# Optimization experiments

Measured on AMD Instinct MI355X. Metric: run time of the kernel, lower is better.

## Reference

```python
import jax, jax.numpy as jnp
import numpy as np
from jax import lax

B, C, T, D, H, W = 1, 8, 8, 24, 48, 48
KT = 3  # temporal kernel taps (module's time loop == valid forward conv, stride 1, pad 0)
KS = 3  # spatial kernel size
S = 2   # spatial stride of the transposed conv
P = 1   # spatial padding of the transposed conv


def setup_inputs() -> dict:
    key = jax.random.key(0)
    kx, kw = jax.random.split(key)
    x = jax.random.normal(kx, (B, C, T, D, H, W), dtype=jnp.float32)
    # torch layout (out_channels, in_channels, kT, kD, kH, kW); the module assigns the
    # slice weight[:, :, i] directly as ConvTranspose3d.weight, so at runtime dim0 acts
    # as the transpose-conv INPUT-channel dim (works because in_ch == out_ch).
    fan_in = C * KT * KS ** 3
    bound = float(1.0 / np.sqrt(fan_in))
    weight = jax.random.uniform(kw, (C, C, KT, KS, KS, KS), dtype=jnp.float32,
                                minval=-bound, maxval=bound)
    return {"x": x, "weight": weight}


def _convT3d(x5, wt):
    # x5: [N, Cin, D, H, W]; wt: ConvTranspose3d weight laid out [Cin, Cout, kD, kH, kW].
    # Transposed conv == forward conv with spatially flipped kernel, swapped I/O dims,
    # lhs dilation = stride, per-side padding = dil*(k-1) - p.
    rhs = jnp.flip(wt, axis=(2, 3, 4)).transpose(1, 0, 2, 3, 4)  # [Cout, Cin, k, k, k]
    pad = KS - 1 - P
    return lax.conv_general_dilated(
        x5, rhs,
        window_strides=(1, 1, 1),
        padding=[(pad, pad)] * 3,
        lhs_dilation=(S, S, S),
        dimension_numbers=("NCDHW", "OIDHW", "NCDHW"))


def reference(x, weight):
    b, c, t = x.shape[:3]
    t_o = t - (KT - 1)  # temporal valid forward conv: out[f] = sum_i conv_i(x[f + i])
    # fold time into batch so each temporal tap is a single big 3D conv
    xr = x.transpose(0, 2, 1, 3, 4, 5).reshape(b * t, c, *x.shape[3:])
    out = None
    for i in range(KT):  # small fixed loop over kernel taps
        y = _convT3d(xr, weight[:, :, i])                 # [b*t, C, Do, Ho, Wo]
        y = y.reshape(b, t, *y.shape[1:])[:, i:i + t_o]   # frames x[f+i] -> out[f]
        out = y if out is None else out + y
    return out.transpose(0, 2, 1, 3, 4, 5)  # [B, C, t_o, Do, Ho, Wo]
```

## Files before the change

### kernel.cpp

```cpp
#include <hip/hip_runtime.h>


typedef float  f32x4  __attribute__((ext_vector_type(4)));
typedef float  f4a    __attribute__((ext_vector_type(4)));
typedef short  bf16x8 __attribute__((ext_vector_type(8)));
typedef unsigned int u32;
typedef u32    u32x2  __attribute__((ext_vector_type(2)));
typedef u32    u32x4  __attribute__((ext_vector_type(4)));

namespace {
constexpr int T_ = 8, D_ = 24, H_ = 48, W_ = 48;
constexpr int TO = 6, DO_ = 47, HO = 95, WO = 95;
constexpr int XCS = T_ * D_ * H_ * W_;
constexpr int XFS = D_ * H_ * W_;
constexpr int XDS = H_ * W_;
constexpr long OCS = (long)TO * DO_ * HO * WO;
constexpr int OFS = DO_ * HO * WO;
constexpr int ODS = HO * WO;

constexpr int AG[4] = {24, 12, 12, 8};
constexpr int AOFF[4] = {0, 3072, 4608, 6144};
constexpr int NRSTR = 242;

__global__ __launch_bounds__(256) void pack_kernel(const float* __restrict__ w,
                                                   unsigned short* __restrict__ A) {
  const int tid = blockIdx.x * 256 + threadIdx.x;
  const int nthr = gridDim.x * 256;
  const int KR[4] = {192, 96, 96, 48};
  for (int c = 0; c < 4; ++c) {
    const int cnt = AG[c] * 128;
    for (int e = tid; e < cnt; e += nthr) {
      const int j = e & 7, r = (e >> 3) & 15, g = e >> 7;
      const int k = g * 8 + j;
      float v = 0.f;
      if (k < KR[c]) {
        int gg = -1, kd = 1, kh = 1;
        const int cc = j & 1;
        if (c == 0)      { gg = g;               kd = ((j >> 1) & 1) ? 2 : 0; kh = ((j >> 2) & 1) ? 0 : 2; }
        else if (c == 1) { gg = 2 * g + (j >> 2); kd = ((j >> 1) & 1) ? 2 : 0; kh = 1; }
        else if (c == 2) { gg = 2 * g + (j >> 2); kd = 1; kh = ((j >> 1) & 1) ? 0 : 2; }
        else             { gg = 4 * g + (j >> 1); kd = 1; kh = 1; }
        if (gg >= 0 && gg < 24) {
          const int ci = gg / 3, i = gg - 3 * (gg / 3);
          const int co = r & 7;
          int kw = (r < 8) ? (cc == 0 ? 1 : -1) : (cc == 0 ? 2 : 0);
          if (kw >= 0) v = w[ci * 648 + co * 81 + i * 27 + kd * 9 + kh * 3 + kw];
        }
      }
      u32 u = __float_as_uint(v);
      u += 0x7FFFu + ((u >> 16) & 1u);
      A[AOFF[c] + e] = (unsigned short)(u >> 16);
    }
  }
}

__device__ __forceinline__ int rowb(int gg, int dl) {
  const int ci = gg / 3;
  return (ci * 5 + (gg - 3 * ci) + dl) * 6;
}

template<int PD, int PH>
__device__ __forceinline__ void wave_body(
    const u32* __restrict__ lds, const unsigned short* __restrict__ A,
    float* __restrict__ out, int f0, int od, int oh, int ihb, int lane)
{
  constexpr int CLS = (PD && PH) ? 0 : PD ? 1 : PH ? 2 : 3;
  constexpr int NSTEP = (CLS == 0) ? 6 : (CLS == 3) ? 2 : 3;
  const int c15 = lane & 15, q = lane >> 4;
  const int th = ((oh + PH) >> 1) - ihb;

  bf16x8 af[NSTEP];
  {
    const unsigned short* Ap = A + AOFF[CLS] + c15 * 8;
    #pragma unroll
    for (int s = 0; s < NSTEP; ++s)
      af[s] = *reinterpret_cast<const bf16x8*>(Ap + (s * 4 + q) * 128);
  }

  const int isO = (q >= 2);
  const int co0 = (q & 1) * 4;

  #pragma unroll
  for (int dl = 0; dl < 3; ++dl) {
    f32x4 acc[3];
    #pragma unroll
    for (int b = 0; b < 3; ++b) acc[b] = {0, 0, 0, 0};

    #pragma unroll
    for (int blk = 0; blk < 3; ++blk) {
      const int n = blk * 16 + c15;
      const u32* col = lds + n * NRSTR;
      #pragma unroll
      for (int s = 0; s < NSTEP; ++s) {
        const int G = s * 4 + q;
        u32x4 ue;
        if constexpr (CLS == 0) {
          const u32* b = col + rowb(G, dl) + 2 * th - 2;
          const u32x2 lo = *reinterpret_cast<const u32x2*>(b);
          const u32x2 hi = *reinterpret_cast<const u32x2*>(b + 2);
          ue = u32x4{lo.x, lo.y, hi.x, hi.y};
        } else if constexpr (CLS == 1) {
          const u32* b0 = col + rowb(2 * G, dl) + 2 * th;
          const u32* b1 = col + rowb(2 * G + 1, dl) + 2 * th;
          const u32x2 lo = *reinterpret_cast<const u32x2*>(b0);
          const u32x2 hi = *reinterpret_cast<const u32x2*>(b1);
          ue = u32x4{lo.x, lo.y, hi.x, hi.y};
        } else if constexpr (CLS == 2) {
          const int r0 = rowb(2 * G, dl), r1 = rowb(2 * G + 1, dl);
          ue = u32x4{col[r0 + 2 * th - 1], col[r0 + 2 * th + 1],
                     col[r1 + 2 * th - 1], col[r1 + 2 * th + 1]};
        } else {
          #pragma unroll
          for (int d = 0; d < 4; ++d) {
            int gg = 4 * G + d; gg = (gg > 23) ? 23 : gg;
            ue[d] = col[rowb(gg, dl) + 2 * th + 1];
          }
        }
        acc[blk] = __builtin_amdgcn_mfma_f32_16x16x32_bf16(af[s], __builtin_bit_cast(bf16x8, ue), acc[blk], 0, 0, 0);
      }
    }

    #pragma unroll
    for (int blk = 0; blk < 3; ++blk) {
      const int ow = blk * 32 + 2 * c15 + isO;
      if (ow < 95) {
        const long ob = (long)(f0 + dl) * OFS + (long)od * ODS + (long)oh * HO + ow;
        #pragma unroll
        for (int j = 0; j < 4; ++j)
          out[(long)(co0 + j) * OCS + ob] = acc[blk][j];
      }
    }
  }
}

constexpr int NBLK = 2 * 24 * 24;

__global__ __launch_bounds__(512) void convt4d_kernel(
    const float* __restrict__ x, const unsigned short* __restrict__ A,
    float* __restrict__ out)
{
  __shared__ u32 lds[48 * NRSTR];

  constexpr int qq = NBLK / 8;
  const int bid = blockIdx.x;
  const int L = (bid & 7) * qq + (bid >> 3);
  const int og = L % 24;
  const int rest = L / 24;
  const int odp = rest % 24, fp = rest / 24;
  const int f0 = 3 * fp;

  const int tid = threadIdx.x;
  const int ihb = og * 2;
  const int idp = odp + 1;

  for (int c = tid; c < 240 * 12; c += 512) {
    const int row = c / 12, ch = c % 12;
    const int ggp = row / 6;
    const int rem = row % 6;
    const int t = rem >> 1, e = rem & 1;
    const int ci = ggp / 5, fi = ggp % 5;
    int plane = idp - e; if (plane > 23) plane = 23;
    int ih = ihb + t; if (ih > 47) ih = 47;
    const float* src = x + ci * XCS + (f0 + fi) * XFS + plane * XDS + ih * W_ + ch * 4;
    const f4a v = *reinterpret_cast<const f4a*>(src);
    const float v4 = (ch == 11) ? 0.f : src[4];
    const u32 b0 = __float_as_uint(v.x), b1 = __float_as_uint(v.y);
    const u32 b2 = __float_as_uint(v.z), b3 = __float_as_uint(v.w);
    const u32 b4 = __float_as_uint(v4);
    u32* dst = lds + (4 * ch) * NRSTR + row;
    dst[0 * NRSTR] = __builtin_amdgcn_perm(b1, b0, 0x07060302u);
    dst[1 * NRSTR] = __builtin_amdgcn_perm(b2, b1, 0x07060302u);
    dst[2 * NRSTR] = __builtin_amdgcn_perm(b3, b2, 0x07060302u);
    dst[3 * NRSTR] = __builtin_amdgcn_perm(b4, b3, 0x07060302u);
  }
  __syncthreads();

  const int w = tid >> 6, lane = tid & 63;
  const int half = w >> 2;
  const int od = 2 * odp + half;
  if (od > 46) return;
  int oh = og * 4 + (w & 3);
  if (oh > 94) oh = 93;
  if (half) {
    if (oh & 1) wave_body<1, 1>(lds, A, out, f0, od, oh, ihb, lane);
    else        wave_body<1, 0>(lds, A, out, f0, od, oh, ihb, lane);
  } else {
    if (oh & 1) wave_body<0, 1>(lds, A, out, f0, od, oh, ihb, lane);
    else        wave_body<0, 0>(lds, A, out, f0, od, oh, ihb, lane);
  }
}
}

extern "C" void kernel_launch(void* const* d_in, const int* in_sizes, int n_in,
                              void* d_out, int out_size, void* d_ws, size_t ws_size,
                              hipStream_t stream) {
  const float* x = (const float*)d_in[0];
  const float* w = (const float*)d_in[1];
  float* out = (float*)d_out;
  unsigned short* A = (unsigned short*)d_ws;
  hipLaunchKernelGGL(pack_kernel, dim3(8), dim3(256), 0, stream, w, A);
  hipLaunchKernelGGL(convt4d_kernel, dim3(NBLK), dim3(512), 0, stream, x, A, out);
}
```

Before: 31.74 us.

## Halve output-row tile per block and restructure LDS staging per row

Each block now covers two output rows instead of four, giving twice as many 256-thread blocks. The LDS tile holds only two input rows per plane, so the row offset becomes a compile-time constant per parity class. The staging loop is reworked so each thread loads a whole input row as twelve float4s and writes all 48 shifted bf16 pairs into LDS. The aim is more blocks and more occupancy from a smaller LDS footprint and simpler addressing. The cost is more redundant halo reads from global memory, and per-thread row loads that coalesce less well.

```diff
diff --git a/kernel.cpp b/kernel.cpp
--- a/kernel.cpp
+++ b/kernel.cpp
@@ -20,7 +20,7 @@
 
 constexpr int AG[4] = {24, 12, 12, 8};
 constexpr int AOFF[4] = {0, 3072, 4608, 6144};
-constexpr int NRSTR = 242;
+constexpr int NRSTR = 162;
 
 __global__ __launch_bounds__(256) void pack_kernel(const float* __restrict__ w,
                                                    unsigned short* __restrict__ A) {
@@ -56,18 +56,18 @@
 
 __device__ __forceinline__ int rowb(int gg, int dl) {
   const int ci = gg / 3;
-  return (ci * 5 + (gg - 3 * ci) + dl) * 6;
+  return (ci * 5 + (gg - 3 * ci) + dl) * 4;
 }
 
 template<int PD, int PH>
 __device__ __forceinline__ void wave_body(
     const u32* __restrict__ lds, const unsigned short* __restrict__ A,
-    float* __restrict__ out, int f0, int od, int oh, int ihb, int lane)
+    float* __restrict__ out, int f0, int od, int oh, int lane)
 {
   constexpr int CLS = (PD && PH) ? 0 : PD ? 1 : PH ? 2 : 3;
   constexpr int NSTEP = (CLS == 0) ? 6 : (CLS == 3) ? 2 : 3;
+  constexpr int TH = PH;
   const int c15 = lane & 15, q = lane >> 4;
-  const int th = ((oh + PH) >> 1) - ihb;
 
   bf16x8 af[NSTEP];
   {
@@ -95,25 +95,25 @@
         const int G = s * 4 + q;
         u32x4 ue;
         if constexpr (CLS == 0) {
-          const u32* b = col + rowb(G, dl) + 2 * th - 2;
+          const u32* b = col + rowb(G, dl) + 2 * TH - 2;
           const u32x2 lo = *reinterpret_cast<const u32x2*>(b);
           const u32x2 hi = *reinterpret_cast<const u32x2*>(b + 2);
           ue = u32x4{lo.x, lo.y, hi.x, hi.y};
         } else if constexpr (CLS == 1) {
-          const u32* b0 = col + rowb(2 * G, dl) + 2 * th;
-          const u32* b1 = col + rowb(2 * G + 1, dl) + 2 * th;
+          const u32* b0 = col + rowb(2 * G, dl) + 2 * TH;
+          const u32* b1 = col + rowb(2 * G + 1, dl) + 2 * TH;
           const u32x2 lo = *reinterpret_cast<const u32x2*>(b0);
           const u32x2 hi = *reinterpret_cast<const u32x2*>(b1);
           ue = u32x4{lo.x, lo.y, hi.x, hi.y};
         } else if constexpr (CLS == 2) {
           const int r0 = rowb(2 * G, dl), r1 = rowb(2 * G + 1, dl);
-          ue = u32x4{col[r0 + 2 * th - 1], col[r0 + 2 * th + 1],
-                     col[r1 + 2 * th - 1], col[r1 + 2 * th + 1]};
+          ue = u32x4{col[r0 + 2 * TH - 1], col[r0 + 2 * TH + 1],
+                     col[r1 + 2 * TH - 1], col[r1 + 2 * TH + 1]};
         } else {
           #pragma unroll
           for (int d = 0; d < 4; ++d) {
             int gg = 4 * G + d; gg = (gg > 23) ? 23 : gg;
-            ue[d] = col[rowb(gg, dl) + 2 * th + 1];
+            ue[d] = col[rowb(gg, dl) + 2 * TH + 1];
           }
         }
         acc[blk] = __builtin_amdgcn_mfma_f32_16x16x32_bf16(af[s], __builtin_bit_cast(bf16x8, ue), acc[blk], 0, 0, 0);
@@ -133,9 +133,9 @@
   }
 }
 
-constexpr int NBLK = 2 * 24 * 24;
-
-__global__ __launch_bounds__(512) void convt4d_kernel(
+constexpr int NBLK = 2 * 24 * 48;
+
+__global__ __launch_bounds__(256) void convt4d_kernel(
     const float* __restrict__ x, const unsigned short* __restrict__ A,
     float* __restrict__ out)
 {
@@ -144,49 +144,52 @@
   constexpr int qq = NBLK / 8;
   const int bid = blockIdx.x;
   const int L = (bid & 7) * qq + (bid >> 3);
-  const int og = L % 24;
-  const int rest = L / 24;
+  const int og2 = L % 48;
+  const int rest = L / 48;
   const int odp = rest % 24, fp = rest / 24;
   const int f0 = 3 * fp;
 
   const int tid = threadIdx.x;
-  const int ihb = og * 2;
   const int idp = odp + 1;
 
-  for (int c = tid; c < 240 * 12; c += 512) {
-    const int row = c / 12, ch = c % 12;
-    const int ggp = row / 6;
-    const int rem = row % 6;
+  for (int row = tid; row < 160; row += 256) {
+    const int ggp = row >> 2;
+    const int rem = row & 3;
     const int t = rem >> 1, e = rem & 1;
     const int ci = ggp / 5, fi = ggp % 5;
     int plane = idp - e; if (plane > 23) plane = 23;
-    int ih = ihb + t; if (ih > 47) ih = 47;
-    const float* src = x + ci * XCS + (f0 + fi) * XFS + plane * XDS + ih * W_ + ch * 4;
-    const f4a v = *reinterpret_cast<const f4a*>(src);
-    const float v4 = (ch == 11) ? 0.f : src[4];
-    const u32 b0 = __float_as_uint(v.x), b1 = __float_as_uint(v.y);
-    const u32 b2 = __float_as_uint(v.z), b3 = __float_as_uint(v.w);
-    const u32 b4 = __float_as_uint(v4);
-    u32* dst = lds + (4 * ch) * NRSTR + row;
-    dst[0 * NRSTR] = __builtin_amdgcn_perm(b1, b0, 0x07060302u);
-    dst[1 * NRSTR] = __builtin_amdgcn_perm(b2, b1, 0x07060302u);
-    dst[2 * NRSTR] = __builtin_amdgcn_perm(b3, b2, 0x07060302u);
-    dst[3 * NRSTR] = __builtin_amdgcn_perm(b4, b3, 0x07060302u);
+    int ih = og2 + t; if (ih > 47) ih = 47;
+    const float* src = x + ci * XCS + (f0 + fi) * XFS + plane * XDS + ih * W_;
+    f32x4 v[12];
+    #pragma unroll
+    for (int ch = 0; ch < 12; ++ch)
+      v[ch] = *reinterpret_cast<const f4a*>(src + ch * 4);
+    u32* dst = lds + row;
+    #pragma unroll
+    for (int ch = 0; ch < 12; ++ch) {
+      const u32 b0 = __float_as_uint(v[ch].x), b1 = __float_as_uint(v[ch].y);
+      const u32 b2 = __float_as_uint(v[ch].z), b3 = __float_as_uint(v[ch].w);
+      const u32 b4 = (ch == 11) ? 0u : __float_as_uint(v[ch + 1].x);
+      dst[(4 * ch + 0) * NRSTR] = __builtin_amdgcn_perm(b1, b0, 0x07060302u);
+      dst[(4 * ch + 1) * NRSTR] = __builtin_amdgcn_perm(b2, b1, 0x07060302u);
+      dst[(4 * ch + 2) * NRSTR] = __builtin_amdgcn_perm(b3, b2, 0x07060302u);
+      dst[(4 * ch + 3) * NRSTR] = __builtin_amdgcn_perm(b4, b3, 0x07060302u);
+    }
   }
   __syncthreads();
 
   const int w = tid >> 6, lane = tid & 63;
-  const int half = w >> 2;
+  const int half = w >> 1;
   const int od = 2 * odp + half;
   if (od > 46) return;
-  int oh = og * 4 + (w & 3);
-  if (oh > 94) oh = 93;
+  int oh = og2 * 2 + (w & 1);
+  if (oh > 94) oh = 94;
   if (half) {
-    if (oh & 1) wave_body<1, 1>(lds, A, out, f0, od, oh, ihb, lane);
-    else        wave_body<1, 0>(lds, A, out, f0, od, oh, ihb, lane);
+    if (oh & 1) wave_body<1, 1>(lds, A, out, f0, od, oh, lane);
+    else        wave_body<1, 0>(lds, A, out, f0, od, oh, lane);
   } else {
-    if (oh & 1) wave_body<0, 1>(lds, A, out, f0, od, oh, ihb, lane);
-    else        wave_body<0, 0>(lds, A, out, f0, od, oh, ihb, lane);
+    if (oh & 1) wave_body<0, 1>(lds, A, out, f0, od, oh, lane);
+    else        wave_body<0, 0>(lds, A, out, f0, od, oh, lane);
   }
 }
 }
@@ -199,5 +202,5 @@
   float* out = (float*)d_out;
   unsigned short* A = (unsigned short*)d_ws;
   hipLaunchKernelGGL(pack_kernel, dim3(8), dim3(256), 0, stream, w, A);
-  hipLaunchKernelGGL(convt4d_kernel, dim3(NBLK), dim3(512), 0, stream, x, A, out);
-}
+  hipLaunchKernelGGL(convt4d_kernel, dim3(NBLK), dim3(256), 0, stream, x, A, out);
+}
```

Measured after the change: 30.30 us. 4.5% less time.
